# Performance work log

Hardware: AMD Instinct MI355X
Metric: run time of the kernel (lower is better)

Reference implementation:

```python
import jax, jax.numpy as jnp
import numpy as np

WINDOW_SIZE = 11
SIGMA = 1.5
DATA_RANGE = 1.0
WEIGHTS = np.array([0.0448, 0.2856, 0.3001, 0.2363, 0.1333], dtype=np.float32)


def _gaussian_window(window_size, sigma, channels, dtype):
    coords = jnp.arange(window_size, dtype=jnp.float32) - window_size // 2
    g = jnp.exp(-(coords ** 2) / (2.0 * sigma ** 2))
    g = g / g.sum()
    w2d = jnp.outer(g, g)  # (K, K)
    # depthwise kernel, OIHW with I=1, O=channels
    return jnp.broadcast_to(w2d, (channels, 1, window_size, window_size)).astype(dtype)


def _dwconv(x, w, channels, pad):
    return jax.lax.conv_general_dilated(
        x, w, window_strides=(1, 1), padding=[(pad, pad), (pad, pad)],
        dimension_numbers=("NCHW", "OIHW", "NCHW"), feature_group_count=channels)


def _avg_pool2(x):
    b, c, h, w = x.shape
    return x.reshape(b, c, h // 2, 2, w // 2, 2).mean(axis=(3, 5))


def setup_inputs() -> dict:
    key = jax.random.key(0)
    k1, k2 = jax.random.split(key)
    shape = (16, 3, 512, 512)
    pred = jax.random.uniform(k1, shape, dtype=jnp.float32)
    target = jax.random.uniform(k2, shape, dtype=jnp.float32)
    return {"pred": pred, "target": target}


def reference(pred, target):
    weights = jnp.asarray(WEIGHTS, dtype=pred.dtype)
    levels = weights.shape[0]
    channels = pred.shape[1]
    pad = WINDOW_SIZE // 2
    window = _gaussian_window(WINDOW_SIZE, SIGMA, channels, pred.dtype)
    C1 = (0.01 * DATA_RANGE) ** 2
    C2 = (0.03 * DATA_RANGE) ** 2

    mcs_vals = []
    msssim_last = None
    for i in range(levels):
        mu_p = _dwconv(pred, window, channels, pad)
        mu_t = _dwconv(target, window, channels, pad)
        mu_pp = mu_p ** 2
        mu_tt = mu_t ** 2
        mu_pt = mu_p * mu_t
        sig_pp = _dwconv(pred ** 2, window, channels, pad) - mu_pp
        sig_tt = _dwconv(target ** 2, window, channels, pad) - mu_tt
        sig_pt = _dwconv(pred * target, window, channels, pad) - mu_pt
        luminance = (2.0 * mu_pt + C1) / (mu_pp + mu_tt + C1)
        cs = (2.0 * sig_pt + C2) / (sig_pp + sig_tt + C2)
        if i == levels - 1:
            msssim_last = (luminance * cs).mean()
        else:
            mcs_vals.append(cs.mean())
        pred = _avg_pool2(pred)
        target = _avg_pool2(target)

    msssim = msssim_last
    for i, mcs in enumerate(mcs_vals):
        msssim = msssim * mcs ** weights[i]
    return 1.0 - msssim
```

## Files before the change

kernel.cpp:

```cpp
#include <hip/hip_runtime.h>
#include <math.h>


#define NIMG 48
#define TWO_C1 2.0e-4f
#define TWO_C2 1.8e-3f

struct CInfo { int base[5]; int cnt[5]; };

#define FOR11(X) X(0) X(1) X(2) X(3) X(4) X(5) X(6) X(7) X(8) X(9) X(10)

#define TAPLOAD_I(K) \
  const float p##K = rpl_[K]; const float t##K = rtl_[K];
#define TAPLOAD_M(K) \
  float p##K, t##K; { \
    const int x_ = gx + (K) - 5; \
    const int xc_ = min(max(x_, 0), W - 1); \
    const float pv_ = rp_[xc_], tv_ = rt_[xc_]; \
    const bool ok_ = ((unsigned)x_ < (unsigned)W); \
    p##K = ok_ ? pv_ : 0.f; t##K = ok_ ? tv_ : 0.f; }

#define HACC(K) { \
    const float a_ = p##K + t##K, b_ = p##K - t##K; \
    hA_ = __builtin_fmaf(G##K, a_, hA_); \
    hB_ = __builtin_fmaf(G##K, b_, hB_); \
    hP_ = __builtin_fmaf(G##K * a_, a_, hP_); \
    hQ_ = __builtin_fmaf(G##K * b_, b_, hQ_); }

#define DECLR(K) float rA##K = 0.f, rB##K = 0.f, rP##K = 0.f, rQ##K = 0.f;

#define MS_STEP_N(R, SW) do { \
    const int r_ = (R); \
    float hA_ = 0.f, hB_ = 0.f, hP_ = 0.f, hQ_ = 0.f; \
    float pc_ = 0.f, tc_ = 0.f; \
    if ((unsigned)r_ < (unsigned)H) { \
      const float* rp_ = Pi + (size_t)r_ * W; \
      const float* rt_ = Ti + (size_t)r_ * W; \
      if (MASKED) { \
        FOR11(TAPLOAD_M) \
        FOR11(HACC) \
        pc_ = p5; tc_ = t5; \
      } else { \
        const float* rpl_ = rp_ + gx - 5; \
        const float* rtl_ = rt_ + gx - 5; \
        FOR11(TAPLOAD_I) \
        FOR11(HACC) \
        pc_ = p5; tc_ = t5; \
      } \
    } \
    rA##SW = hA_; rB##SW = hB_; rP##SW = hP_; rQ##SW = hQ_; \
    if (DS) { \
      if (r_ >= y0 && r_ < y0 + nout) { \
        if ((r_ & 1) == 0) { pr = pc_; tr = tc_; } \
        else { \
          float sp_ = pr + pc_, st_ = tr + tc_; \
          sp_ += __shfl_xor(sp_, 1, 64); \
          st_ += __shfl_xor(st_, 1, 64); \
          if ((lane & 1) == 0) { \
            const size_t o_ = obase + (size_t)(r_ >> 1) * (W >> 1) + \
                              (size_t)(gx >> 1); \
            dsP[o_] = sp_ * 0.25f; \
            dsT[o_] = st_ * 0.25f; \
          } } } } \
  } while (0)

#define VSTEP(GK, S) \
    A_ = __builtin_fmaf(GK, rA##S, A_); B_ = __builtin_fmaf(GK, rB##S, B_); \
    P_ = __builtin_fmaf(GK, rP##S, P_); Q_ = __builtin_fmaf(GK, rQ##S, Q_);

#define ROW_N(IROW, SW, S0,S1,S2,S3,S4,S5,S6,S7,S8,S9,S10) do { \
    const int i_ = (IROW); \
    const bool live_ = (i_ < nout); \
    MS_STEP_N(y0 + 5 + i_, SW); \
    float A_ = G0 * rA##S0, B_ = G0 * rB##S0; \
    float P_ = G0 * rP##S0, Q_ = G0 * rQ##S0; \
    VSTEP(G1, S1) VSTEP(G2, S2) VSTEP(G3, S3) VSTEP(G4, S4) VSTEP(G5, S5) \
    VSTEP(G6, S6) VSTEP(G7, S7) VSTEP(G8, S8) VSTEP(G9, S9) VSTEP(G10, S10) \
    const float A2_ = A_ * A_, B2_ = B_ * B_; \
    const float dAB_ = A2_ - B2_, sAB_ = A2_ + B2_; \
    const float cn_ = (P_ - Q_) - dAB_ + TWO_C2; \
    const float cd_ = (P_ + Q_) - sAB_ + TWO_C2; \
    float val_; \
    if (LAST) val_ = ((dAB_ + TWO_C1) * cn_) / ((sAB_ + TWO_C1) * cd_); \
    else      val_ = cn_ / cd_; \
    if ((!MASKED || gx < W) && live_) sum += val_; \
  } while (0)

template <int MASKED, int DS, int LAST>
__device__ __forceinline__ float strip_run(
    const float* __restrict__ Pi, const float* __restrict__ Ti,
    const int H, const int W, const int y0, const int nout, const int c0,
    float* __restrict__ dsP, float* __restrict__ dsT, const size_t obase,
    const float G0, const float G1, const float G2, const float G3,
    const float G4, const float G5, const float G6, const float G7,
    const float G8, const float G9, const float G10) {
  const int lane = threadIdx.x & 63;
  const int gx = c0 + lane;
  FOR11(DECLR)
  float pr = 0.f, tr = 0.f, sum = 0.f;

  MS_STEP_N(y0 - 5, 0); MS_STEP_N(y0 - 4, 1); MS_STEP_N(y0 - 3, 2);
  MS_STEP_N(y0 - 2, 3); MS_STEP_N(y0 - 1, 4); MS_STEP_N(y0 + 0, 5);
  MS_STEP_N(y0 + 1, 6); MS_STEP_N(y0 + 2, 7); MS_STEP_N(y0 + 3, 8);
  MS_STEP_N(y0 + 4, 9);

  for (int base = 0; base < nout; base += 11) {
    ROW_N(base + 0, 10, 0,1,2,3,4,5,6,7,8,9,10);
    ROW_N(base + 1, 0,  1,2,3,4,5,6,7,8,9,10,0);
    ROW_N(base + 2, 1,  2,3,4,5,6,7,8,9,10,0,1);
    ROW_N(base + 3, 2,  3,4,5,6,7,8,9,10,0,1,2);
    ROW_N(base + 4, 3,  4,5,6,7,8,9,10,0,1,2,3);
    ROW_N(base + 5, 4,  5,6,7,8,9,10,0,1,2,3,4);
    ROW_N(base + 6, 5,  6,7,8,9,10,0,1,2,3,4,5);
    ROW_N(base + 7, 6,  7,8,9,10,0,1,2,3,4,5,6);
    ROW_N(base + 8, 7,  8,9,10,0,1,2,3,4,5,6,7);
    ROW_N(base + 9, 8,  9,10,0,1,2,3,4,5,6,7,8);
    ROW_N(base + 10, 9, 10,0,1,2,3,4,5,6,7,8,9);
  }
  return sum;
}

template <int DS, int LAST>
__global__ __launch_bounds__(256, 3)
void msssim_level_k(const float* __restrict__ P, const float* __restrict__ T,
                    const int H, const int W, const int strips,
                    const int chunks, const int chunkH, const int tasks,
                    float* __restrict__ dsP, float* __restrict__ dsT,
                    double* __restrict__ partial,
                    const float G0, const float G1, const float G2,
                    const float G3, const float G4, const float G5,
                    const float G6, const float G7, const float G8,
                    const float G9, const float G10) {
  __shared__ float sRed[4];
  const int tid = threadIdx.x;
  const int lane = tid & 63;
  const int wid = tid >> 6;
  float sum = 0.f;
  const int task = blockIdx.x * 4 + wid;
  if (task < tasks) {
    const int strip = task % strips;
    const int rem = task / strips;
    const int chunk = rem % chunks;
    const int img = rem / chunks;
    const int y0 = chunk * chunkH;
    const int nout = min(chunkH, H - y0);
    const size_t ibase = (size_t)img * H * W;
    const size_t obase = DS ? (size_t)img * (size_t)(H >> 1) * (W >> 1) : 0;
    const bool edge = (strip == 0) || (strip * 64 + 69 > W);
    if (edge)
      sum = strip_run<1, DS, LAST>(P + ibase, T + ibase, H, W, y0, nout,
                                   strip * 64, dsP, dsT, obase,
                                   G0, G1, G2, G3, G4, G5, G6, G7, G8, G9, G10);
    else
      sum = strip_run<0, DS, LAST>(P + ibase, T + ibase, H, W, y0, nout,
                                   strip * 64, dsP, dsT, obase,
                                   G0, G1, G2, G3, G4, G5, G6, G7, G8, G9, G10);
  }
#pragma unroll
  for (int off = 32; off; off >>= 1) sum += __shfl_down(sum, off, 64);
  if (lane == 0) sRed[wid] = sum;
  __syncthreads();
  if (tid == 0)
    partial[blockIdx.x] = (double)(sRed[0] + sRed[1] + sRed[2] + sRed[3]);
}

__global__ void msssim_combine_k(const double* __restrict__ partial,
                                 float* __restrict__ out, const CInfo ci) {
  const int lane = threadIdx.x & 63;
  double lv[5];
#pragma unroll
  for (int L = 0; L < 5; ++L) {
    double s = 0.0;
    for (int i = lane; i < ci.cnt[L]; i += 64) s += partial[ci.base[L] + i];
#pragma unroll
    for (int off = 32; off; off >>= 1) s += __shfl_down(s, off, 64);
    lv[L] = s;
  }
  if (lane == 0) {
    double ms = lv[4] / (48.0 * 32.0 * 32.0);
    ms *= pow(lv[0] / (48.0 * 512.0 * 512.0), (double)0.0448f);
    ms *= pow(lv[1] / (48.0 * 256.0 * 256.0), (double)0.2856f);
    ms *= pow(lv[2] / (48.0 * 128.0 * 128.0), (double)0.3001f);
    ms *= pow(lv[3] / (48.0 * 64.0 * 64.0),  (double)0.2363f);
    out[0] = (float)(1.0 - ms);
  }
}

extern "C" void kernel_launch(void* const* d_in, const int* in_sizes, int n_in,
                              void* d_out, int out_size, void* d_ws, size_t ws_size,
                              hipStream_t stream) {
  const float* pred = (const float*)d_in[0];
  const float* targ = (const float*)d_in[1];
  float* out = (float*)d_out;

  char* ws = (char*)d_ws;
  double* partial = (double*)ws;
  size_t off = 32768;
  auto alloc = [&](size_t elems) {
    float* p = (float*)(ws + off);
    off += elems * sizeof(float);
    return p;
  };
  float* L1p = alloc((size_t)NIMG * 256 * 256);
  float* L1t = alloc((size_t)NIMG * 256 * 256);
  float* L2p = alloc((size_t)NIMG * 128 * 128);
  float* L2t = alloc((size_t)NIMG * 128 * 128);
  float* L3p = alloc((size_t)NIMG * 64 * 64);
  float* L3t = alloc((size_t)NIMG * 64 * 64);
  float* L4p = alloc((size_t)NIMG * 32 * 32);
  float* L4t = alloc((size_t)NIMG * 32 * 32);

  float g[11];
  {
    double gd[11], s = 0.0;
    for (int k = 0; k < 11; ++k) {
      const double c = (double)(k - 5);
      gd[k] = exp(-(c * c) / 4.5);
      s += gd[k];
    }
    for (int k = 0; k < 11; ++k) g[k] = (float)(gd[k] / s);
  }

  CInfo ci;
  int slotOff = 0;

  auto launchLevel = [&](const float* P, const float* T, int H, int W,
                         int chunkH, float* dP, float* dT, int L, bool last) {
    const int strips = (W + 63) / 64;
    const int chunks = (H + chunkH - 1) / chunkH;
    const int tasks = strips * chunks * NIMG;
    const int blocks = (tasks + 3) / 4;
    ci.base[L] = slotOff;
    ci.cnt[L] = blocks;
    if (last) {
      msssim_level_k<0, 1><<<blocks, 256, 0, stream>>>(
          P, T, H, W, strips, chunks, chunkH, tasks, nullptr, nullptr,
          partial + slotOff, g[0], g[1], g[2], g[3], g[4], g[5], g[6], g[7],
          g[8], g[9], g[10]);
    } else {
      msssim_level_k<1, 0><<<blocks, 256, 0, stream>>>(
          P, T, H, W, strips, chunks, chunkH, tasks, dP, dT,
          partial + slotOff, g[0], g[1], g[2], g[3], g[4], g[5], g[6], g[7],
          g[8], g[9], g[10]);
    }
    slotOff += blocks;
  };

  launchLevel(pred, targ, 512, 512, 32, L1p, L1t, 0, false);
  launchLevel(L1p, L1t, 256, 256, 32, L2p, L2t, 1, false);
  launchLevel(L2p, L2t, 128, 128, 32, L3p, L3t, 2, false);
  launchLevel(L3p, L3t, 64, 64, 16, L4p, L4t, 3, false);
  launchLevel(L4p, L4t, 32, 32, 8, nullptr, nullptr, 4, true);

  msssim_combine_k<<<1, 64, 0, stream>>>(partial, out, ci);
}
```

Measured before the change: 219.1 us.

## Swap filter order: vertical first, horizontal via ds_bpermute with halo lanes

Each lane now loads one pixel per row and does the vertical 11-tap pass in registers. The horizontal pass exchanges the four vertical sums across lanes with ds_bpermute. Strips overlap, so each 64-lane wave produces 52 valid output columns and 12 lanes serve as halo. This replaces 22 scattered global loads per row with 2 coalesced loads, at the cost of 40 LDS permutes per row and about 19% redundant lanes. The chunk height is fixed at 32 with full unrolling and launch bounds move to 4 waves per EU. This fixed height makes chunk counting assume H is divisible by 32, which breaks the 32x32 level (chunks=1 fine) but 64x64 now uses 2 chunks.

```diff
diff --git a/kernel.cpp b/kernel.cpp
--- a/kernel.cpp
+++ b/kernel.cpp
@@ -3,6 +3,8 @@
 
 
 #define NIMG 48
+#define OUTW 52
+#define CH 32
 #define TWO_C1 2.0e-4f
 #define TWO_C2 1.8e-3f
 
@@ -10,54 +12,33 @@
 
 #define FOR11(X) X(0) X(1) X(2) X(3) X(4) X(5) X(6) X(7) X(8) X(9) X(10)
 
-#define TAPLOAD_I(K) \
-  const float p##K = rpl_[K]; const float t##K = rtl_[K];
-#define TAPLOAD_M(K) \
-  float p##K, t##K; { \
-    const int x_ = gx + (K) - 5; \
-    const int xc_ = min(max(x_, 0), W - 1); \
-    const float pv_ = rp_[xc_], tv_ = rt_[xc_]; \
-    const bool ok_ = ((unsigned)x_ < (unsigned)W); \
-    p##K = ok_ ? pv_ : 0.f; t##K = ok_ ? tv_ : 0.f; }
-
-#define HACC(K) { \
-    const float a_ = p##K + t##K, b_ = p##K - t##K; \
-    hA_ = __builtin_fmaf(G##K, a_, hA_); \
-    hB_ = __builtin_fmaf(G##K, b_, hB_); \
-    hP_ = __builtin_fmaf(G##K * a_, a_, hP_); \
-    hQ_ = __builtin_fmaf(G##K * b_, b_, hQ_); }
-
 #define DECLR(K) float rA##K = 0.f, rB##K = 0.f, rP##K = 0.f, rQ##K = 0.f;
+#define DECLIDX(K) const int ix##K = (lane + (K) - 5) * 4;
+
+__device__ __forceinline__ float bperm_f(int idx, float v) {
+  return __int_as_float(__builtin_amdgcn_ds_bpermute(idx, __float_as_int(v)));
+}
 
 #define MS_STEP_N(R, SW) do { \
     const int r_ = (R); \
-    float hA_ = 0.f, hB_ = 0.f, hP_ = 0.f, hQ_ = 0.f; \
-    float pc_ = 0.f, tc_ = 0.f; \
-    if ((unsigned)r_ < (unsigned)H) { \
-      const float* rp_ = Pi + (size_t)r_ * W; \
-      const float* rt_ = Ti + (size_t)r_ * W; \
-      if (MASKED) { \
-        FOR11(TAPLOAD_M) \
-        FOR11(HACC) \
-        pc_ = p5; tc_ = t5; \
-      } else { \
-        const float* rpl_ = rp_ + gx - 5; \
-        const float* rtl_ = rt_ + gx - 5; \
-        FOR11(TAPLOAD_I) \
-        FOR11(HACC) \
-        pc_ = p5; tc_ = t5; \
-      } \
-    } \
-    rA##SW = hA_; rB##SW = hB_; rP##SW = hP_; rQ##SW = hQ_; \
+    const float pC = pN, tC = tN; \
+    { const int rn_ = r_ + 1; \
+      pN = 0.f; tN = 0.f; \
+      if (((unsigned)rn_ < (unsigned)H) && colv) { \
+        const size_t ro_ = (size_t)rn_ * W + (size_t)gx; \
+        pN = Pi[ro_]; tN = Ti[ro_]; \
+      } } \
+    const float aC = pC + tC, bC = pC - tC; \
+    rA##SW = aC; rB##SW = bC; rP##SW = aC * aC; rQ##SW = bC * bC; \
     if (DS) { \
-      if (r_ >= y0 && r_ < y0 + nout) { \
-        if ((r_ & 1) == 0) { pr = pc_; tr = tc_; } \
+      if (r_ >= y0 && r_ < y0 + CH) { \
+        if ((r_ & 1) == 0) { pr = pC; tr = tC; } \
         else { \
-          float sp_ = pr + pc_, st_ = tr + tc_; \
+          float sp_ = pr + pC, st_ = tr + tC; \
           sp_ += __shfl_xor(sp_, 1, 64); \
           st_ += __shfl_xor(st_, 1, 64); \
-          if ((lane & 1) == 0) { \
-            const size_t o_ = obase + (size_t)(r_ >> 1) * (W >> 1) + \
+          if (((lane & 1) == 0) && outl) { \
+            const size_t o_ = obase + (size_t)(r_ >> 1) * (size_t)(W >> 1) + \
                               (size_t)(gx >> 1); \
             dsP[o_] = sp_ * 0.25f; \
             dsT[o_] = st_ * 0.25f; \
@@ -65,66 +46,68 @@
   } while (0)
 
 #define VSTEP(GK, S) \
-    A_ = __builtin_fmaf(GK, rA##S, A_); B_ = __builtin_fmaf(GK, rB##S, B_); \
-    P_ = __builtin_fmaf(GK, rP##S, P_); Q_ = __builtin_fmaf(GK, rQ##S, Q_);
+    vA_ = __builtin_fmaf(GK, rA##S, vA_); vB_ = __builtin_fmaf(GK, rB##S, vB_); \
+    vP_ = __builtin_fmaf(GK, rP##S, vP_); vQ_ = __builtin_fmaf(GK, rQ##S, vQ_);
+
+#define HTAP(K) { \
+    const float ta_ = bperm_f(ix##K, vA_); \
+    const float tb_ = bperm_f(ix##K, vB_); \
+    const float tp_ = bperm_f(ix##K, vP_); \
+    const float tq_ = bperm_f(ix##K, vQ_); \
+    hA_ = __builtin_fmaf(G##K, ta_, hA_); \
+    hB_ = __builtin_fmaf(G##K, tb_, hB_); \
+    hP_ = __builtin_fmaf(G##K, tp_, hP_); \
+    hQ_ = __builtin_fmaf(G##K, tq_, hQ_); }
 
 #define ROW_N(IROW, SW, S0,S1,S2,S3,S4,S5,S6,S7,S8,S9,S10) do { \
-    const int i_ = (IROW); \
-    const bool live_ = (i_ < nout); \
-    MS_STEP_N(y0 + 5 + i_, SW); \
-    float A_ = G0 * rA##S0, B_ = G0 * rB##S0; \
-    float P_ = G0 * rP##S0, Q_ = G0 * rQ##S0; \
+    MS_STEP_N(y0 + 5 + (IROW), SW); \
+    float vA_ = G0 * rA##S0, vB_ = G0 * rB##S0; \
+    float vP_ = G0 * rP##S0, vQ_ = G0 * rQ##S0; \
     VSTEP(G1, S1) VSTEP(G2, S2) VSTEP(G3, S3) VSTEP(G4, S4) VSTEP(G5, S5) \
     VSTEP(G6, S6) VSTEP(G7, S7) VSTEP(G8, S8) VSTEP(G9, S9) VSTEP(G10, S10) \
-    const float A2_ = A_ * A_, B2_ = B_ * B_; \
+    float hA_ = G5 * vA_, hB_ = G5 * vB_, hP_ = G5 * vP_, hQ_ = G5 * vQ_; \
+    HTAP(0) HTAP(1) HTAP(2) HTAP(3) HTAP(4) \
+    HTAP(6) HTAP(7) HTAP(8) HTAP(9) HTAP(10) \
+    const float A2_ = hA_ * hA_, B2_ = hB_ * hB_; \
     const float dAB_ = A2_ - B2_, sAB_ = A2_ + B2_; \
-    const float cn_ = (P_ - Q_) - dAB_ + TWO_C2; \
-    const float cd_ = (P_ + Q_) - sAB_ + TWO_C2; \
+    const float cn_ = (hP_ - hQ_) - dAB_ + TWO_C2; \
+    const float cd_ = (hP_ + hQ_) - sAB_ + TWO_C2; \
     float val_; \
     if (LAST) val_ = ((dAB_ + TWO_C1) * cn_) / ((sAB_ + TWO_C1) * cd_); \
     else      val_ = cn_ / cd_; \
-    if ((!MASKED || gx < W) && live_) sum += val_; \
+    if (outl) sum += val_; \
   } while (0)
 
-template <int MASKED, int DS, int LAST>
-__device__ __forceinline__ float strip_run(
-    const float* __restrict__ Pi, const float* __restrict__ Ti,
-    const int H, const int W, const int y0, const int nout, const int c0,
-    float* __restrict__ dsP, float* __restrict__ dsT, const size_t obase,
-    const float G0, const float G1, const float G2, const float G3,
-    const float G4, const float G5, const float G6, const float G7,
-    const float G8, const float G9, const float G10) {
-  const int lane = threadIdx.x & 63;
-  const int gx = c0 + lane;
-  FOR11(DECLR)
-  float pr = 0.f, tr = 0.f, sum = 0.f;
-
-  MS_STEP_N(y0 - 5, 0); MS_STEP_N(y0 - 4, 1); MS_STEP_N(y0 - 3, 2);
-  MS_STEP_N(y0 - 2, 3); MS_STEP_N(y0 - 1, 4); MS_STEP_N(y0 + 0, 5);
-  MS_STEP_N(y0 + 1, 6); MS_STEP_N(y0 + 2, 7); MS_STEP_N(y0 + 3, 8);
-  MS_STEP_N(y0 + 4, 9);
-
-  for (int base = 0; base < nout; base += 11) {
-    ROW_N(base + 0, 10, 0,1,2,3,4,5,6,7,8,9,10);
-    ROW_N(base + 1, 0,  1,2,3,4,5,6,7,8,9,10,0);
-    ROW_N(base + 2, 1,  2,3,4,5,6,7,8,9,10,0,1);
-    ROW_N(base + 3, 2,  3,4,5,6,7,8,9,10,0,1,2);
-    ROW_N(base + 4, 3,  4,5,6,7,8,9,10,0,1,2,3);
-    ROW_N(base + 5, 4,  5,6,7,8,9,10,0,1,2,3,4);
-    ROW_N(base + 6, 5,  6,7,8,9,10,0,1,2,3,4,5);
-    ROW_N(base + 7, 6,  7,8,9,10,0,1,2,3,4,5,6);
-    ROW_N(base + 8, 7,  8,9,10,0,1,2,3,4,5,6,7);
-    ROW_N(base + 9, 8,  9,10,0,1,2,3,4,5,6,7,8);
-    ROW_N(base + 10, 9, 10,0,1,2,3,4,5,6,7,8,9);
-  }
-  return sum;
-}
+#define BLOCK11(BASE) \
+    ROW_N((BASE) + 0, 10, 0,1,2,3,4,5,6,7,8,9,10); \
+    ROW_N((BASE) + 1, 0,  1,2,3,4,5,6,7,8,9,10,0); \
+    ROW_N((BASE) + 2, 1,  2,3,4,5,6,7,8,9,10,0,1); \
+    ROW_N((BASE) + 3, 2,  3,4,5,6,7,8,9,10,0,1,2); \
+    ROW_N((BASE) + 4, 3,  4,5,6,7,8,9,10,0,1,2,3); \
+    ROW_N((BASE) + 5, 4,  5,6,7,8,9,10,0,1,2,3,4); \
+    ROW_N((BASE) + 6, 5,  6,7,8,9,10,0,1,2,3,4,5); \
+    ROW_N((BASE) + 7, 6,  7,8,9,10,0,1,2,3,4,5,6); \
+    ROW_N((BASE) + 8, 7,  8,9,10,0,1,2,3,4,5,6,7); \
+    ROW_N((BASE) + 9, 8,  9,10,0,1,2,3,4,5,6,7,8); \
+    ROW_N((BASE) + 10, 9, 10,0,1,2,3,4,5,6,7,8,9);
+
+#define BLOCK10(BASE) \
+    ROW_N((BASE) + 0, 10, 0,1,2,3,4,5,6,7,8,9,10); \
+    ROW_N((BASE) + 1, 0,  1,2,3,4,5,6,7,8,9,10,0); \
+    ROW_N((BASE) + 2, 1,  2,3,4,5,6,7,8,9,10,0,1); \
+    ROW_N((BASE) + 3, 2,  3,4,5,6,7,8,9,10,0,1,2); \
+    ROW_N((BASE) + 4, 3,  4,5,6,7,8,9,10,0,1,2,3); \
+    ROW_N((BASE) + 5, 4,  5,6,7,8,9,10,0,1,2,3,4); \
+    ROW_N((BASE) + 6, 5,  6,7,8,9,10,0,1,2,3,4,5); \
+    ROW_N((BASE) + 7, 6,  7,8,9,10,0,1,2,3,4,5,6); \
+    ROW_N((BASE) + 8, 7,  8,9,10,0,1,2,3,4,5,6,7); \
+    ROW_N((BASE) + 9, 8,  9,10,0,1,2,3,4,5,6,7,8);
 
 template <int DS, int LAST>
-__global__ __launch_bounds__(256, 3)
+__global__ __launch_bounds__(256, 4)
 void msssim_level_k(const float* __restrict__ P, const float* __restrict__ T,
                     const int H, const int W, const int strips,
-                    const int chunks, const int chunkH, const int tasks,
+                    const int chunks, const int tasks,
                     float* __restrict__ dsP, float* __restrict__ dsT,
                     double* __restrict__ partial,
                     const float G0, const float G1, const float G2,
@@ -142,20 +125,37 @@
     const int rem = task / strips;
     const int chunk = rem % chunks;
     const int img = rem / chunks;
-    const int y0 = chunk * chunkH;
-    const int nout = min(chunkH, H - y0);
-    const size_t ibase = (size_t)img * H * W;
+    const int y0 = chunk * CH;
+    const int gx = strip * OUTW + lane - 6;
+    const bool colv = ((unsigned)gx < (unsigned)W);
+    const bool outl = (lane >= 6) && (lane < 58) && colv;
+    const float* Pi = P + (size_t)img * H * W;
+    const float* Ti = T + (size_t)img * H * W;
     const size_t obase = DS ? (size_t)img * (size_t)(H >> 1) * (W >> 1) : 0;
-    const bool edge = (strip == 0) || (strip * 64 + 69 > W);
-    if (edge)
-      sum = strip_run<1, DS, LAST>(P + ibase, T + ibase, H, W, y0, nout,
-                                   strip * 64, dsP, dsT, obase,
-                                   G0, G1, G2, G3, G4, G5, G6, G7, G8, G9, G10);
-    else
-      sum = strip_run<0, DS, LAST>(P + ibase, T + ibase, H, W, y0, nout,
-                                   strip * 64, dsP, dsT, obase,
-                                   G0, G1, G2, G3, G4, G5, G6, G7, G8, G9, G10);
-  }
+
+    FOR11(DECLR)
+    FOR11(DECLIDX)
+    float pr = 0.f, tr = 0.f;
+    float pN = 0.f, tN = 0.f;
+
+    {
+      const int r0 = y0 - 5;
+      if (((unsigned)r0 < (unsigned)H) && colv) {
+        const size_t ro = (size_t)r0 * W + (size_t)gx;
+        pN = Pi[ro]; tN = Ti[ro];
+      }
+    }
+
+    MS_STEP_N(y0 - 5, 0); MS_STEP_N(y0 - 4, 1); MS_STEP_N(y0 - 3, 2);
+    MS_STEP_N(y0 - 2, 3); MS_STEP_N(y0 - 1, 4); MS_STEP_N(y0 + 0, 5);
+    MS_STEP_N(y0 + 1, 6); MS_STEP_N(y0 + 2, 7); MS_STEP_N(y0 + 3, 8);
+    MS_STEP_N(y0 + 4, 9);
+
+    BLOCK11(0)
+    BLOCK11(11)
+    BLOCK10(22)
+  }
+
 #pragma unroll
   for (int off = 32; off; off >>= 1) sum += __shfl_down(sum, off, 64);
   if (lane == 0) sRed[wid] = sum;
@@ -225,32 +225,32 @@
   int slotOff = 0;
 
   auto launchLevel = [&](const float* P, const float* T, int H, int W,
-                         int chunkH, float* dP, float* dT, int L, bool last) {
-    const int strips = (W + 63) / 64;
-    const int chunks = (H + chunkH - 1) / chunkH;
+                         float* dP, float* dT, int L, bool last) {
+    const int strips = (W + OUTW - 1) / OUTW;
+    const int chunks = H / CH;
     const int tasks = strips * chunks * NIMG;
     const int blocks = (tasks + 3) / 4;
     ci.base[L] = slotOff;
     ci.cnt[L] = blocks;
     if (last) {
       msssim_level_k<0, 1><<<blocks, 256, 0, stream>>>(
-          P, T, H, W, strips, chunks, chunkH, tasks, nullptr, nullptr,
+          P, T, H, W, strips, chunks, tasks, nullptr, nullptr,
           partial + slotOff, g[0], g[1], g[2], g[3], g[4], g[5], g[6], g[7],
           g[8], g[9], g[10]);
     } else {
       msssim_level_k<1, 0><<<blocks, 256, 0, stream>>>(
-          P, T, H, W, strips, chunks, chunkH, tasks, dP, dT,
+          P, T, H, W, strips, chunks, tasks, dP, dT,
           partial + slotOff, g[0], g[1], g[2], g[3], g[4], g[5], g[6], g[7],
           g[8], g[9], g[10]);
     }
     slotOff += blocks;
   };
 
-  launchLevel(pred, targ, 512, 512, 32, L1p, L1t, 0, false);
-  launchLevel(L1p, L1t, 256, 256, 32, L2p, L2t, 1, false);
-  launchLevel(L2p, L2t, 128, 128, 32, L3p, L3t, 2, false);
-  launchLevel(L3p, L3t, 64, 64, 16, L4p, L4t, 3, false);
-  launchLevel(L4p, L4t, 32, 32, 8, nullptr, nullptr, 4, true);
+  launchLevel(pred, targ, 512, 512, L1p, L1t, 0, false);
+  launchLevel(L1p, L1t, 256, 256, L2p, L2t, 1, false);
+  launchLevel(L2p, L2t, 128, 128, L3p, L3t, 2, false);
+  launchLevel(L3p, L3t, 64, 64, L4p, L4t, 3, false);
+  launchLevel(L4p, L4t, 32, 32, nullptr, nullptr, 4, true);
 
   msssim_combine_k<<<1, 64, 0, stream>>>(partial, out, ci);
 }
```

New measurement: 258.8 us. 18.1% more time.

## Add guard-free interior strip path and enlarge row chunks per task

Applied to the files above, without the earlier changes.

Adds a strip_safe path for interior strips whose whole row range is in bounds. It drops the per-row bounds checks, issues the next row's loads before finishing the current output row, and overlaps the vertical sum with the horizontal pass of the new row. The chunk height grows at every level, which cuts the redundant 10-row halo recompute per task but leaves fewer tasks and so less parallelism. A gx<W guard is also added to the downsample store.

```diff
diff --git a/kernel.cpp b/kernel.cpp
--- a/kernel.cpp
+++ b/kernel.cpp
@@ -9,6 +9,29 @@
 struct CInfo { int base[5]; int cnt[5]; };
 
 #define FOR11(X) X(0) X(1) X(2) X(3) X(4) X(5) X(6) X(7) X(8) X(9) X(10)
+
+#define DECLR(K) float rA##K = 0.f, rB##K = 0.f, rP##K = 0.f, rQ##K = 0.f;
+
+#define HACC(K) { \
+    const float a_ = p##K + t##K; \
+    const float b_ = p##K - t##K; \
+    hA_ = __builtin_fmaf(G##K, a_, hA_); \
+    hB_ = __builtin_fmaf(G##K, b_, hB_); \
+    hP_ = __builtin_fmaf(G##K * a_, a_, hP_); \
+    hQ_ = __builtin_fmaf(G##K * b_, b_, hQ_); }
+
+#define VSTEP(GK, S) \
+    vA_ = __builtin_fmaf(GK, rA##S, vA_); vB_ = __builtin_fmaf(GK, rB##S, vB_); \
+    vP_ = __builtin_fmaf(GK, rP##S, vP_); vQ_ = __builtin_fmaf(GK, rQ##S, vQ_);
+
+#define SSIM_STATS \
+    const float A2_ = vA_ * vA_, B2_ = vB_ * vB_; \
+    const float dAB_ = A2_ - B2_, sAB_ = A2_ + B2_; \
+    const float cn_ = (vP_ - vQ_) - dAB_ + TWO_C2; \
+    const float cd_ = (vP_ + vQ_) - sAB_ + TWO_C2; \
+    float val_; \
+    if (LAST) val_ = ((dAB_ + TWO_C1) * cn_) / ((sAB_ + TWO_C1) * cd_); \
+    else      val_ = cn_ / cd_;
 
 #define TAPLOAD_I(K) \
   const float p##K = rpl_[K]; const float t##K = rtl_[K];
@@ -19,15 +42,6 @@
     const float pv_ = rp_[xc_], tv_ = rt_[xc_]; \
     const bool ok_ = ((unsigned)x_ < (unsigned)W); \
     p##K = ok_ ? pv_ : 0.f; t##K = ok_ ? tv_ : 0.f; }
-
-#define HACC(K) { \
-    const float a_ = p##K + t##K, b_ = p##K - t##K; \
-    hA_ = __builtin_fmaf(G##K, a_, hA_); \
-    hB_ = __builtin_fmaf(G##K, b_, hB_); \
-    hP_ = __builtin_fmaf(G##K * a_, a_, hP_); \
-    hQ_ = __builtin_fmaf(G##K * b_, b_, hQ_); }
-
-#define DECLR(K) float rA##K = 0.f, rB##K = 0.f, rP##K = 0.f, rQ##K = 0.f;
 
 #define MS_STEP_N(R, SW) do { \
     const int r_ = (R); \
@@ -56,38 +70,28 @@
           float sp_ = pr + pc_, st_ = tr + tc_; \
           sp_ += __shfl_xor(sp_, 1, 64); \
           st_ += __shfl_xor(st_, 1, 64); \
-          if ((lane & 1) == 0) { \
-            const size_t o_ = obase + (size_t)(r_ >> 1) * (W >> 1) + \
+          if (((lane & 1) == 0) && (gx < W)) { \
+            const size_t o_ = obase + (size_t)(r_ >> 1) * (size_t)(W >> 1) + \
                               (size_t)(gx >> 1); \
             dsP[o_] = sp_ * 0.25f; \
             dsT[o_] = st_ * 0.25f; \
           } } } } \
   } while (0)
 
-#define VSTEP(GK, S) \
-    A_ = __builtin_fmaf(GK, rA##S, A_); B_ = __builtin_fmaf(GK, rB##S, B_); \
-    P_ = __builtin_fmaf(GK, rP##S, P_); Q_ = __builtin_fmaf(GK, rQ##S, Q_);
-
-#define ROW_N(IROW, SW, S0,S1,S2,S3,S4,S5,S6,S7,S8,S9,S10) do { \
+#define ROW_G(IROW, SW, S0,S1,S2,S3,S4,S5,S6,S7,S8,S9) do { \
     const int i_ = (IROW); \
     const bool live_ = (i_ < nout); \
     MS_STEP_N(y0 + 5 + i_, SW); \
-    float A_ = G0 * rA##S0, B_ = G0 * rB##S0; \
-    float P_ = G0 * rP##S0, Q_ = G0 * rQ##S0; \
+    float vA_ = G0 * rA##S0, vB_ = G0 * rB##S0; \
+    float vP_ = G0 * rP##S0, vQ_ = G0 * rQ##S0; \
     VSTEP(G1, S1) VSTEP(G2, S2) VSTEP(G3, S3) VSTEP(G4, S4) VSTEP(G5, S5) \
-    VSTEP(G6, S6) VSTEP(G7, S7) VSTEP(G8, S8) VSTEP(G9, S9) VSTEP(G10, S10) \
-    const float A2_ = A_ * A_, B2_ = B_ * B_; \
-    const float dAB_ = A2_ - B2_, sAB_ = A2_ + B2_; \
-    const float cn_ = (P_ - Q_) - dAB_ + TWO_C2; \
-    const float cd_ = (P_ + Q_) - sAB_ + TWO_C2; \
-    float val_; \
-    if (LAST) val_ = ((dAB_ + TWO_C1) * cn_) / ((sAB_ + TWO_C1) * cd_); \
-    else      val_ = cn_ / cd_; \
+    VSTEP(G6, S6) VSTEP(G7, S7) VSTEP(G8, S8) VSTEP(G9, S9) VSTEP(G10, SW) \
+    SSIM_STATS \
     if ((!MASKED || gx < W) && live_) sum += val_; \
   } while (0)
 
 template <int MASKED, int DS, int LAST>
-__device__ __forceinline__ float strip_run(
+__device__ __forceinline__ float strip_guard(
     const float* __restrict__ Pi, const float* __restrict__ Ti,
     const int H, const int W, const int y0, const int nout, const int c0,
     float* __restrict__ dsP, float* __restrict__ dsT, const size_t obase,
@@ -105,17 +109,97 @@
   MS_STEP_N(y0 + 4, 9);
 
   for (int base = 0; base < nout; base += 11) {
-    ROW_N(base + 0, 10, 0,1,2,3,4,5,6,7,8,9,10);
-    ROW_N(base + 1, 0,  1,2,3,4,5,6,7,8,9,10,0);
-    ROW_N(base + 2, 1,  2,3,4,5,6,7,8,9,10,0,1);
-    ROW_N(base + 3, 2,  3,4,5,6,7,8,9,10,0,1,2);
-    ROW_N(base + 4, 3,  4,5,6,7,8,9,10,0,1,2,3);
-    ROW_N(base + 5, 4,  5,6,7,8,9,10,0,1,2,3,4);
-    ROW_N(base + 6, 5,  6,7,8,9,10,0,1,2,3,4,5);
-    ROW_N(base + 7, 6,  7,8,9,10,0,1,2,3,4,5,6);
-    ROW_N(base + 8, 7,  8,9,10,0,1,2,3,4,5,6,7);
-    ROW_N(base + 9, 8,  9,10,0,1,2,3,4,5,6,7,8);
-    ROW_N(base + 10, 9, 10,0,1,2,3,4,5,6,7,8,9);
+    ROW_G(base + 0, 10, 0,1,2,3,4,5,6,7,8,9);
+    ROW_G(base + 1, 0,  1,2,3,4,5,6,7,8,9,10);
+    ROW_G(base + 2, 1,  2,3,4,5,6,7,8,9,10,0);
+    ROW_G(base + 3, 2,  3,4,5,6,7,8,9,10,0,1);
+    ROW_G(base + 4, 3,  4,5,6,7,8,9,10,0,1,2);
+    ROW_G(base + 5, 4,  5,6,7,8,9,10,0,1,2,3);
+    ROW_G(base + 6, 5,  6,7,8,9,10,0,1,2,3,4);
+    ROW_G(base + 7, 6,  7,8,9,10,0,1,2,3,4,5);
+    ROW_G(base + 8, 7,  8,9,10,0,1,2,3,4,5,6);
+    ROW_G(base + 9, 8,  9,10,0,1,2,3,4,5,6,7);
+    ROW_G(base + 10, 9, 10,0,1,2,3,4,5,6,7,8);
+  }
+  return sum;
+}
+
+#define SLD(K) \
+  const float p##K = rpl_[K]; const float t##K = rtl_[K];
+
+#define SDS(PC, TC) \
+    if (DS) { \
+      if (r_ < y0 + nout) { \
+        if ((r_ & 1) == 0) { pr = (PC); tr = (TC); } \
+        else { \
+          float sp_ = pr + (PC), st_ = tr + (TC); \
+          sp_ += __shfl_xor(sp_, 1, 64); \
+          st_ += __shfl_xor(st_, 1, 64); \
+          if ((lane & 1) == 0) { \
+            const size_t o_ = obase + (size_t)(r_ >> 1) * (size_t)(W >> 1) + \
+                              (size_t)(gx >> 1); \
+            dsP[o_] = sp_ * 0.25f; \
+            dsT[o_] = st_ * 0.25f; \
+          } } } }
+
+#define SPRO(RR, SW) do { \
+    const int r_ = (RR); \
+    const float* rpl_ = Pi + (size_t)r_ * W + gx - 5; \
+    const float* rtl_ = Ti + (size_t)r_ * W + gx - 5; \
+    FOR11(SLD) \
+    float hA_ = 0.f, hB_ = 0.f, hP_ = 0.f, hQ_ = 0.f; \
+    FOR11(HACC) \
+    rA##SW = hA_; rB##SW = hB_; rP##SW = hP_; rQ##SW = hQ_; \
+    if (r_ >= y0) { SDS(p5, t5) } \
+  } while (0)
+
+#define ROW_S(JJ, S0,S1,S2,S3,S4,S5,S6,S7,S8,S9,S10) do { \
+    const int i_ = base + (JJ); \
+    const int r_ = y0 + 5 + i_; \
+    const float* rpl_ = Pi + (size_t)r_ * W + gx - 5; \
+    const float* rtl_ = Ti + (size_t)r_ * W + gx - 5; \
+    FOR11(SLD) \
+    float vA_ = G0 * rA##S0, vB_ = G0 * rB##S0; \
+    float vP_ = G0 * rP##S0, vQ_ = G0 * rQ##S0; \
+    VSTEP(G1, S1) VSTEP(G2, S2) VSTEP(G3, S3) VSTEP(G4, S4) VSTEP(G5, S5) \
+    VSTEP(G6, S6) VSTEP(G7, S7) VSTEP(G8, S8) VSTEP(G9, S9) VSTEP(G10, S10) \
+    SSIM_STATS \
+    if ((i_ >= 1) && (i_ - 1 < nout)) sum += val_; \
+    float hA_ = 0.f, hB_ = 0.f, hP_ = 0.f, hQ_ = 0.f; \
+    FOR11(HACC) \
+    rA##S0 = hA_; rB##S0 = hB_; rP##S0 = hP_; rQ##S0 = hQ_; \
+    SDS(p5, t5) \
+  } while (0)
+
+template <int DS, int LAST>
+__device__ __forceinline__ float strip_safe(
+    const float* __restrict__ Pi, const float* __restrict__ Ti,
+    const int H, const int W, const int y0, const int nout, const int c0,
+    float* __restrict__ dsP, float* __restrict__ dsT, const size_t obase,
+    const float G0, const float G1, const float G2, const float G3,
+    const float G4, const float G5, const float G6, const float G7,
+    const float G8, const float G9, const float G10) {
+  const int lane = threadIdx.x & 63;
+  const int gx = c0 + lane;
+  FOR11(DECLR)
+  float pr = 0.f, tr = 0.f, sum = 0.f;
+
+  SPRO(y0 - 5, 1); SPRO(y0 - 4, 2); SPRO(y0 - 3, 3); SPRO(y0 - 2, 4);
+  SPRO(y0 - 1, 5); SPRO(y0 + 0, 6); SPRO(y0 + 1, 7); SPRO(y0 + 2, 8);
+  SPRO(y0 + 3, 9); SPRO(y0 + 4, 10);
+
+  for (int base = 0; base < nout + 1; base += 11) {
+    ROW_S(0,  0,1,2,3,4,5,6,7,8,9,10);
+    ROW_S(1,  1,2,3,4,5,6,7,8,9,10,0);
+    ROW_S(2,  2,3,4,5,6,7,8,9,10,0,1);
+    ROW_S(3,  3,4,5,6,7,8,9,10,0,1,2);
+    ROW_S(4,  4,5,6,7,8,9,10,0,1,2,3);
+    ROW_S(5,  5,6,7,8,9,10,0,1,2,3,4);
+    ROW_S(6,  6,7,8,9,10,0,1,2,3,4,5);
+    ROW_S(7,  7,8,9,10,0,1,2,3,4,5,6);
+    ROW_S(8,  8,9,10,0,1,2,3,4,5,6,7);
+    ROW_S(9,  9,10,0,1,2,3,4,5,6,7,8);
+    ROW_S(10, 10,0,1,2,3,4,5,6,7,8,9);
   }
   return sum;
 }
@@ -146,15 +230,21 @@
     const int nout = min(chunkH, H - y0);
     const size_t ibase = (size_t)img * H * W;
     const size_t obase = DS ? (size_t)img * (size_t)(H >> 1) * (W >> 1) : 0;
-    const bool edge = (strip == 0) || (strip * 64 + 69 > W);
-    if (edge)
-      sum = strip_run<1, DS, LAST>(P + ibase, T + ibase, H, W, y0, nout,
-                                   strip * 64, dsP, dsT, obase,
-                                   G0, G1, G2, G3, G4, G5, G6, G7, G8, G9, G10);
+    const bool edgeS = (strip == 0) || (strip * 64 + 69 > W);
+    const int nbodies = ((nout + 11) / 11) * 11;
+    const bool safeR = (y0 >= 5) && (y0 + 5 + nbodies - 1 < H);
+    if (!edgeS && safeR)
+      sum = strip_safe<DS, LAST>(P + ibase, T + ibase, H, W, y0, nout,
+                                 strip * 64, dsP, dsT, obase,
+                                 G0, G1, G2, G3, G4, G5, G6, G7, G8, G9, G10);
+    else if (!edgeS)
+      sum = strip_guard<0, DS, LAST>(P + ibase, T + ibase, H, W, y0, nout,
+                                     strip * 64, dsP, dsT, obase,
+                                     G0, G1, G2, G3, G4, G5, G6, G7, G8, G9, G10);
     else
-      sum = strip_run<0, DS, LAST>(P + ibase, T + ibase, H, W, y0, nout,
-                                   strip * 64, dsP, dsT, obase,
-                                   G0, G1, G2, G3, G4, G5, G6, G7, G8, G9, G10);
+      sum = strip_guard<1, DS, LAST>(P + ibase, T + ibase, H, W, y0, nout,
+                                     strip * 64, dsP, dsT, obase,
+                                     G0, G1, G2, G3, G4, G5, G6, G7, G8, G9, G10);
   }
 #pragma unroll
   for (int off = 32; off; off >>= 1) sum += __shfl_down(sum, off, 64);
@@ -246,11 +336,11 @@
     slotOff += blocks;
   };
 
-  launchLevel(pred, targ, 512, 512, 32, L1p, L1t, 0, false);
-  launchLevel(L1p, L1t, 256, 256, 32, L2p, L2t, 1, false);
-  launchLevel(L2p, L2t, 128, 128, 32, L3p, L3t, 2, false);
-  launchLevel(L3p, L3t, 64, 64, 16, L4p, L4t, 3, false);
-  launchLevel(L4p, L4t, 32, 32, 8, nullptr, nullptr, 4, true);
+  launchLevel(pred, targ, 512, 512, 64, L1p, L1t, 0, false);
+  launchLevel(L1p, L1t, 256, 256, 64, L2p, L2t, 1, false);
+  launchLevel(L2p, L2t, 128, 128, 64, L3p, L3t, 2, false);
+  launchLevel(L3p, L3t, 64, 64, 64, L4p, L4t, 3, false);
+  launchLevel(L4p, L4t, 32, 32, 32, nullptr, nullptr, 4, true);
 
   msssim_combine_k<<<1, 64, 0, stream>>>(partial, out, ci);
 }
```

After: 564.0 us. +157.4%, slower.
